# Performance work log

Hardware: AMD Instinct MI355X
Metric: run time of the kernel (lower is better)

The kernel has to match this reference:

```python
import jax, jax.numpy as jnp
import numpy as np
from jax import lax

N = 14
K = 512
NUM_CLASSES = 10
TAO = 0.5 / (N * N)
BETA = 2.0


def make_t_p(n=N, tao=TAO, beta=BETA):
    # t_p[i, j, a, b] = tao * max(1 - beta * (|a-i| + |b-j|) / n, -1)
    idx = jnp.arange(n, dtype=jnp.float32)
    d = (jnp.abs(idx[:, None, None, None] - idx[None, None, :, None])
         + jnp.abs(idx[None, :, None, None] - idx[None, None, None, :]))
    return (tao * jnp.maximum(1.0 - beta * d / n, -1.0)).astype(jnp.float32)


def masked_output(x, t_p):
    # Vectorized equivalent of computeMaskedOutput: global spatial argmax per
    # (batch, channel) selects a template, then masked = relu(x * template).
    B, H, W, C = x.shape
    flat_idx = jnp.argmax(x.reshape(B, H * W, C), axis=1)      # [B, C]
    pi, pj = flat_idx // W, flat_idx % W
    tpl = t_p[pi, pj]                                          # [B, C, H, W]
    tpl = jnp.transpose(tpl, (0, 2, 3, 1))                     # [B, H, W, C]
    masked = jax.nn.relu(x * tpl)
    return masked, x, tpl


def compute_loss(x, pos_templates, act_sums, cls_sums, gt):
    # Fused segment-sum form of the original nested python loops.
    classes = jnp.zeros(NUM_CLASSES, x.dtype).at[gt].add(1.0)  # bincount
    cls_new = cls_sums + classes
    means = jnp.mean(x, axis=(1, 2))                           # [B, C]
    onehot = jax.nn.one_hot(gt, NUM_CLASSES, dtype=x.dtype)    # [B, 10]
    act_new = act_sums + means.T @ onehot                      # [C, 10]
    # divide_no_nan
    fm = jnp.where(cls_new[None, :] == 0, 0.0,
                   act_new / jnp.where(cls_new[None, :] == 0, 1.0, cls_new[None, :]))
    fclass = jnp.argmax(fm, axis=1)                            # [C]
    match = fclass[None, :] == gt[:, None]                     # [B, C]
    pt = jax.nn.relu(pos_templates)
    # relu(t_n) == 0 since t_n is strictly negative
    loss = jnp.where(match[:, None, None, :], pt, 0.0)
    return loss, act_new, cls_new


def forward(inputs, gt, conv_w, conv_b, dense_w, dense_b,
            activation_sums_1, activation_sums_2, class_sums_1, class_sums_2):
    t_p = make_t_p()
    raw_map = inputs  # base_model treated as identity on its feature map
    x1, X1_relu, pos_t1 = masked_output(raw_map, t_p)
    x3 = jax.nn.relu(lax.conv_general_dilated(
        x1, conv_w, window_strides=(1, 1), padding='SAME',
        dimension_numbers=('NHWC', 'HWIO', 'NHWC')) + conv_b)
    x2, X2_relu, pos_t2 = masked_output(x3, t_p)
    pooled = lax.reduce_window(x2, -jnp.inf, lax.max,
                               (1, 2, 2, 1), (1, 2, 2, 1), 'VALID')
    flat = pooled.reshape(pooled.shape[0], -1)
    probs = jax.nn.softmax(flat @ dense_w + dense_b, axis=-1)
    loss1, as1, cs1 = compute_loss(x1, pos_t1, activation_sums_1, class_sums_1, gt)
    loss2, as2, cs2 = compute_loss(x2, pos_t2, activation_sums_2, class_sums_2, gt)
    return probs, x1, x2, loss1, loss2, raw_map, pos_t1


def setup_inputs() -> dict:
    key = jax.random.key(0)
    ks = jax.random.split(key, 4)
    B = 128
    inputs = jax.random.uniform(ks[0], (B, N, N, K), dtype=jnp.float32)
    gt = jax.random.randint(ks[1], (B,), 0, NUM_CLASSES)
    conv_w = jax.random.normal(ks[2], (3, 3, K, K), dtype=jnp.float32) * 0.02
    conv_b = jnp.zeros((K,), jnp.float32)
    D = (N // 2) * (N // 2) * K  # 25088
    dense_w = jax.random.normal(ks[3], (D, NUM_CLASSES), dtype=jnp.float32) * 0.02
    dense_b = jnp.zeros((NUM_CLASSES,), jnp.float32)
    return {
        'inputs': inputs, 'gt': gt,
        'conv_w': conv_w, 'conv_b': conv_b,
        'dense_w': dense_w, 'dense_b': dense_b,
        'activation_sums_1': jnp.zeros((K, NUM_CLASSES), jnp.float32),
        'activation_sums_2': jnp.zeros((K, NUM_CLASSES), jnp.float32),
        'class_sums_1': jnp.zeros((NUM_CLASSES,), jnp.float32),
        'class_sums_2': jnp.zeros((NUM_CLASSES,), jnp.float32),
    }


def reference(inputs, gt, conv_w, conv_b, dense_w, dense_b,
              activation_sums_1, activation_sums_2, class_sums_1, class_sums_2):
    return forward(inputs, gt, conv_w, conv_b, dense_w, dense_b,
                   activation_sums_1, activation_sums_2,
                   class_sums_1, class_sums_2)
```

## Files before the change

kernel.cpp:

```cpp
#include <hip/hip_runtime.h>
#include <hip/hip_bf16.h>
#include <stdint.h>

#define TAO_F (0.5f/196.0f)

typedef short s16x8 __attribute__((ext_vector_type(8)));
typedef float f32x4 __attribute__((ext_vector_type(4)));
typedef __attribute__((address_space(1))) const unsigned int u32_g;
typedef __attribute__((address_space(3))) unsigned int u32_l;

__device__ __forceinline__ void async_ld16(const void* g, void* l) {
  __builtin_amdgcn_global_load_lds((u32_g*)g, (u32_l*)l, 16, 0, 0);
}

__global__ void k_prep_w(const float* __restrict__ w, __hip_bfloat16* __restrict__ wT) {
  __shared__ float tile[64][65];
  int bid = blockIdx.x;
  int r = bid / 64; int rem = bid - r * 64;
  int cib = (rem >> 3) * 64, cob = (rem & 7) * 64;
  int tid = threadIdx.x;
  int col = tid & 63, rw = tid >> 6;
#pragma unroll
  for (int p = 0; p < 16; ++p) {
    int row = p * 4 + rw;
    tile[row][col] = w[(size_t)(r * 512 + cib + row) * 512 + cob + col];
  }
  __syncthreads();
#pragma unroll
  for (int p = 0; p < 16; ++p) {
    int row = p * 4 + rw;
    wT[(size_t)(r * 512 + cob + row) * 512 + cib + col] = __float2bfloat16(tile[col][row]);
  }
}

__global__ void k_argmax(const float* __restrict__ src, int* __restrict__ idx,
                         float* __restrict__ rawcopy) {
  int t = blockIdx.x * 256 + threadIdx.x;
  const float* p = src + (size_t)(t >> 9) * 196 * 512 + (t & 511);
  float best = -1e30f; int bi = 0;
  if (rawcopy) {
    float* rp = rawcopy + (size_t)(t >> 9) * 196 * 512 + (t & 511);
    for (int s = 0; s < 196; ++s) {
      float v = p[(size_t)s * 512];
      rp[(size_t)s * 512] = v;
      if (v > best) { best = v; bi = s; }
    }
  } else {
    for (int s = 0; s < 196; ++s) {
      float v = p[(size_t)s * 512];
      if (v > best) { best = v; bi = s; }
    }
  }
  idx[t] = bi;
}

__global__ void k_mask1(const float* __restrict__ in, const int* __restrict__ idx1,
                        const int* __restrict__ gt, float* __restrict__ out_x1,
                        float* __restrict__ out_t1, __hip_bfloat16* __restrict__ x1p,
                        float* __restrict__ act1) {
  int t = blockIdx.x * 256 + threadIdx.x;
  int b = t >> 9, c = t & 511;
  int id = idx1[t];
  int pi = id / 14, pj = id - pi * 14;
  const float* ip = in + (size_t)b * 196 * 512 + c;
  float* ox = out_x1 + (size_t)b * 196 * 512 + c;
  float* ot = out_t1 + (size_t)b * 196 * 512 + c;
  __hip_bfloat16* xp = x1p + ((size_t)(b * 16 + 1) * 16 + 1) * 512 + c;
  float sum = 0.f;
  for (int i = 0; i < 14; ++i) {
    int di = (i > pi) ? (i - pi) : (pi - i);
    for (int j = 0; j < 14; ++j) {
      int d = di + ((j > pj) ? (j - pj) : (pj - j));
      float tpl = TAO_F * fmaxf(1.0f - (float)d / 7.0f, -1.0f);
      float x = ip[(size_t)(i * 14 + j) * 512];
      float m = fmaxf(x * tpl, 0.0f);
      ox[(size_t)(i * 14 + j) * 512] = m;
      ot[(size_t)(i * 14 + j) * 512] = tpl;
      xp[(size_t)(i * 16 + j) * 512] = __float2bfloat16(m);
      sum += m;
    }
  }
  atomicAdd(&act1[c * 10 + gt[b]], sum * (1.0f / 196.0f));
}

__global__ void k_mask2(const float* __restrict__ x3, const int* __restrict__ idx2,
                        const int* __restrict__ gt, float* __restrict__ out_x2,
                        float* __restrict__ act2) {
  int t = blockIdx.x * 256 + threadIdx.x;
  int b = t >> 9, c = t & 511;
  int id = idx2[t];
  int pi = id / 14, pj = id - pi * 14;
  const float* ip = x3 + (size_t)b * 196 * 512 + c;
  float* ox = out_x2 + (size_t)b * 196 * 512 + c;
  float sum = 0.f;
  for (int i = 0; i < 14; ++i) {
    int di = (i > pi) ? (i - pi) : (pi - i);
    for (int j = 0; j < 14; ++j) {
      int d = di + ((j > pj) ? (j - pj) : (pj - j));
      float tpl = TAO_F * fmaxf(1.0f - (float)d / 7.0f, -1.0f);
      float x = ip[(size_t)(i * 14 + j) * 512];
      float m = fmaxf(x * tpl, 0.0f);
      ox[(size_t)(i * 14 + j) * 512] = m;
      sum += m;
    }
  }
  atomicAdd(&act2[c * 10 + gt[b]], sum * (1.0f / 196.0f));
}

__global__ __launch_bounds__(256, 2) void k_gemm(const __hip_bfloat16* __restrict__ x1p,
                                                 const __hip_bfloat16* __restrict__ wT,
                                                 const float* __restrict__ conv_b,
                                                 float* __restrict__ x3) {
  int bid = blockIdx.x;
  int nt4 = bid & 3; int mt196 = bid >> 2;
  int m0 = mt196 * 128, co0 = nt4 * 128;
  int tid = threadIdx.x;
  int lane = tid & 63;

  __shared__ short As[128 * 64];
  __shared__ short Bs[128 * 64];

  int srow = tid >> 3;
  int sslot = tid & 7;
  int sx = ((sslot ^ (srow & 7)) * 8);

  int baseA[4];
#pragma unroll
  for (int p = 0; p < 4; ++p) {
    int m = m0 + p * 32 + srow;
    int b = m / 196; int s = m - b * 196; int i = s / 14; int j = s - i * 14;
    baseA[p] = ((b * 16 + i + 1) * 16 + (j + 1)) * 512;
  }
  int baseB[4];
#pragma unroll
  for (int p = 0; p < 4; ++p) baseB[p] = (co0 + p * 32 + srow) * 512;

  f32x4 acc[4][4] = {};

  int m_off = (tid >> 7) * 64;
  int n_off = ((tid >> 6) & 1) * 64;
  int q = lane >> 4;
  int l16 = lane & 15;

  for (int r = 0; r < 9; ++r) {
    int offr = ((r / 3) * 16 + (r % 3) - 17) * 512;
    int wbase = r * 512 * 512;
    for (int cb = 0; cb < 8; ++cb) {
      int ko = cb * 64;
      __syncthreads();
#pragma unroll
      for (int p = 0; p < 4; ++p) {
        async_ld16(x1p + (baseA[p] + offr + ko + sx),
                   &As[(p * 32 + srow) * 64 + sslot * 8]);
        async_ld16(wT + (wbase + baseB[p] + ko + sx),
                   &Bs[(p * 32 + srow) * 64 + sslot * 8]);
      }
      __syncthreads();
#pragma unroll
      for (int kk = 0; kk < 2; ++kk) {
        s16x8 af[4], bf[4];
#pragma unroll
        for (int tt = 0; tt < 4; ++tt) {
          int rowa = m_off + tt * 16 + l16;
          int sa = (kk * 4 + q) ^ (rowa & 7);
          af[tt] = *(const s16x8*)&As[rowa * 64 + sa * 8];
          int rowb = n_off + tt * 16 + l16;
          int sb = (kk * 4 + q) ^ (rowb & 7);
          bf[tt] = *(const s16x8*)&Bs[rowb * 64 + sb * 8];
        }
#pragma unroll
        for (int mt = 0; mt < 4; ++mt)
#pragma unroll
          for (int nt = 0; nt < 4; ++nt)
            acc[mt][nt] = __builtin_amdgcn_mfma_f32_16x16x32_bf16(af[mt], bf[nt], acc[mt][nt], 0, 0, 0);
      }
    }
  }
#pragma unroll
  for (int nt = 0; nt < 4; ++nt) {
    int col = co0 + n_off + nt * 16 + l16;
    float bias = conv_b[col];
#pragma unroll
    for (int mt = 0; mt < 4; ++mt) {
      int mrow = m0 + m_off + mt * 16 + q * 4;
#pragma unroll
      for (int rg = 0; rg < 4; ++rg) {
        float v = acc[mt][nt][rg] + bias;
        x3[(size_t)(mrow + rg) * 512 + col] = fmaxf(v, 0.0f);
      }
    }
  }
}

__global__ void k_dense(const float* __restrict__ x2, const float* __restrict__ dw,
                        const float* __restrict__ db, float* __restrict__ probs) {
  int b = blockIdx.x, tid = threadIdx.x;
  float a[10] = {0.f,0.f,0.f,0.f,0.f,0.f,0.f,0.f,0.f,0.f};
  for (int d = tid; d < 25088; d += 256) {
    int c = d & 511;
    int sj = d >> 9;
    int ii = sj / 7, jj = sj - ii * 7;
    const float* xb = x2 + ((size_t)(b * 14 + 2 * ii) * 14 + 2 * jj) * 512 + c;
    float p0 = xb[0], p1 = xb[512], p2 = xb[14 * 512], p3 = xb[14 * 512 + 512];
    float pm = fmaxf(fmaxf(p0, p1), fmaxf(p2, p3));
    const float* wr = dw + (size_t)d * 10;
#pragma unroll
    for (int t2 = 0; t2 < 10; ++t2) a[t2] += pm * wr[t2];
  }
  __shared__ float red[10];
  if (tid < 10) red[tid] = 0.f;
  __syncthreads();
  int lane = tid & 63;
#pragma unroll
  for (int t2 = 0; t2 < 10; ++t2) {
    float v = a[t2];
    for (int off = 32; off > 0; off >>= 1) v += __shfl_down(v, off);
    if (lane == 0) atomicAdd(&red[t2], v);
  }
  __syncthreads();
  if (tid == 0) {
    float l[10]; float m = -1e30f;
#pragma unroll
    for (int t2 = 0; t2 < 10; ++t2) { l[t2] = red[t2] + db[t2]; m = fmaxf(m, l[t2]); }
    float s = 0.f;
#pragma unroll
    for (int t2 = 0; t2 < 10; ++t2) { l[t2] = expf(l[t2] - m); s += l[t2]; }
    float inv = 1.0f / s;
#pragma unroll
    for (int t2 = 0; t2 < 10; ++t2) probs[b * 10 + t2] = l[t2] * inv;
  }
}

__global__ void k_stats(const float* __restrict__ act1, const float* __restrict__ act2,
                        const float* __restrict__ as1, const float* __restrict__ as2,
                        const float* __restrict__ cs1, const float* __restrict__ cs2,
                        const int* __restrict__ gt, int* __restrict__ fc1, int* __restrict__ fc2) {
  __shared__ int scnt[10];
  int tid = threadIdx.x;
  if (tid < 10) scnt[tid] = 0;
  __syncthreads();
  if (tid < 128) atomicAdd(&scnt[gt[tid]], 1);
  __syncthreads();
  int c = tid;
  float best1 = -1e30f, best2 = -1e30f; int b1 = 0, b2 = 0;
#pragma unroll
  for (int g = 0; g < 10; ++g) {
    float cnt = (float)scnt[g];
    float cn1 = cs1[g] + cnt;
    float cn2 = cs2[g] + cnt;
    float a1 = act1[c * 10 + g] + as1[c * 10 + g];
    float a2 = act2[c * 10 + g] + as2[c * 10 + g];
    float f1 = (cn1 == 0.f) ? 0.f : a1 / cn1;
    float f2 = (cn2 == 0.f) ? 0.f : a2 / cn2;
    if (f1 > best1) { best1 = f1; b1 = g; }
    if (f2 > best2) { best2 = f2; b2 = g; }
  }
  fc1[c] = b1; fc2[c] = b2;
}

__global__ void k_loss(const int* __restrict__ idx1, const int* __restrict__ idx2,
                       const int* __restrict__ fc1, const int* __restrict__ fc2,
                       const int* __restrict__ gt, float* __restrict__ o1, float* __restrict__ o2) {
  int t = blockIdx.x * 256 + threadIdx.x;
  int b = t >> 9, c = t & 511;
  int g = gt[b];
  bool m1 = (fc1[c] == g), m2 = (fc2[c] == g);
  int i1 = idx1[t], i2 = idx2[t];
  int p1i = i1 / 14, p1j = i1 - p1i * 14;
  int p2i = i2 / 14, p2j = i2 - p2i * 14;
  float* w1 = o1 + (size_t)b * 196 * 512 + c;
  float* w2 = o2 + (size_t)b * 196 * 512 + c;
  for (int i = 0; i < 14; ++i) {
    int d1i = (i > p1i) ? (i - p1i) : (p1i - i);
    int d2i = (i > p2i) ? (i - p2i) : (p2i - i);
    for (int j = 0; j < 14; ++j) {
      int d1 = d1i + ((j > p1j) ? (j - p1j) : (p1j - j));
      int d2 = d2i + ((j > p2j) ? (j - p2j) : (p2j - j));
      float r1 = TAO_F * fmaxf(1.0f - (float)d1 / 7.0f, 0.0f);
      float r2 = TAO_F * fmaxf(1.0f - (float)d2 / 7.0f, 0.0f);
      w1[(size_t)(i * 14 + j) * 512] = m1 ? r1 : 0.0f;
      w2[(size_t)(i * 14 + j) * 512] = m2 ? r2 : 0.0f;
    }
  }
}

extern "C" void kernel_launch(void* const* d_in, const int* in_sizes, int n_in,
                              void* d_out, int out_size, void* d_ws, size_t ws_size,
                              hipStream_t stream) {
  const float* inputs  = (const float*)d_in[0];
  const int*   gt      = (const int*)d_in[1];
  const float* conv_w  = (const float*)d_in[2];
  const float* conv_b  = (const float*)d_in[3];
  const float* dense_w = (const float*)d_in[4];
  const float* dense_b = (const float*)d_in[5];
  const float* as1     = (const float*)d_in[6];
  const float* as2     = (const float*)d_in[7];
  const float* cs1     = (const float*)d_in[8];
  const float* cs2     = (const float*)d_in[9];

  float* out = (float*)d_out;
  const size_t S = 12845056;
  float* o_probs = out;
  float* o_x1  = out + 1280;
  float* o_x2  = o_x1 + S;
  float* o_l1  = o_x2 + S;
  float* o_l2  = o_l1 + S;
  float* o_raw = o_l2 + S;
  float* o_t1  = o_raw + S;

  uint8_t* w8 = (uint8_t*)d_ws;
  __hip_bfloat16* x1p = (__hip_bfloat16*)w8;
  float* x3  = (float*)(w8 + 33554432);
  __hip_bfloat16* wT = (__hip_bfloat16*)(w8 + 84934656);
  int*   idx1 = (int*)(w8 + 89653248);
  int*   idx2 = (int*)(w8 + 89915392);
  float* act1 = (float*)(w8 + 90177536);
  float* act2 = (float*)(w8 + 90198016);
  int*   fc1  = (int*)(w8 + 90218496);
  int*   fc2  = (int*)(w8 + 90220544);

  hipMemsetAsync(x1p, 0, 33554432, stream);
  hipMemsetAsync(act1, 0, 40960, stream);

  k_prep_w<<<576, 256, 0, stream>>>(conv_w, wT);
  k_argmax<<<256, 256, 0, stream>>>(inputs, idx1, o_raw);
  k_mask1 <<<256, 256, 0, stream>>>(inputs, idx1, gt, o_x1, o_t1, x1p, act1);
  k_gemm  <<<784, 256, 0, stream>>>(x1p, wT, conv_b, x3);
  k_argmax<<<256, 256, 0, stream>>>(x3, idx2, nullptr);
  k_mask2 <<<256, 256, 0, stream>>>(x3, idx2, gt, o_x2, act2);
  k_dense <<<128, 256, 0, stream>>>(o_x2, dense_w, dense_b, o_probs);
  k_stats <<<1, 512, 0, stream>>>(act1, act2, as1, as2, cs1, cs2, gt, fc1, fc2);
  k_loss  <<<256, 256, 0, stream>>>(idx1, idx2, fc1, fc2, gt, o_l1, o_l2);
}
```

Measured before the change: 671.3 us.

## Fuse argmax with masking and fold dense layer into second mask pass

Merges the argmax and masking kernels for both stages so each thread scans its channel column once for the argmax and then re-reads it for the mask, avoiding a separate launch and idx round-trip. The second fused kernel also does the 2x2 maxpool and dense matvec in registers, accumulating logits atomically so o_x2 is never re-read. Softmax moves into k_stats, and the GEMM launch bound is raised to 3 blocks per SM, which may force register spills. Dense weights are now read per channel-thread with stride-10 access, and float atomics on logits make the summation order nondeterministic.

After: 623.9 us. -7.1%, faster.

```diff
diff --git a/kernel.cpp b/kernel.cpp
--- a/kernel.cpp
+++ b/kernel.cpp
@@ -33,38 +33,24 @@
   }
 }
 
-__global__ void k_argmax(const float* __restrict__ src, int* __restrict__ idx,
-                         float* __restrict__ rawcopy) {
-  int t = blockIdx.x * 256 + threadIdx.x;
-  const float* p = src + (size_t)(t >> 9) * 196 * 512 + (t & 511);
-  float best = -1e30f; int bi = 0;
-  if (rawcopy) {
-    float* rp = rawcopy + (size_t)(t >> 9) * 196 * 512 + (t & 511);
-    for (int s = 0; s < 196; ++s) {
-      float v = p[(size_t)s * 512];
-      rp[(size_t)s * 512] = v;
-      if (v > best) { best = v; bi = s; }
-    }
-  } else {
-    for (int s = 0; s < 196; ++s) {
-      float v = p[(size_t)s * 512];
-      if (v > best) { best = v; bi = s; }
-    }
-  }
-  idx[t] = bi;
-}
-
-__global__ void k_mask1(const float* __restrict__ in, const int* __restrict__ idx1,
-                        const int* __restrict__ gt, float* __restrict__ out_x1,
-                        float* __restrict__ out_t1, __hip_bfloat16* __restrict__ x1p,
-                        float* __restrict__ act1) {
+__global__ void k_fuse1(const float* __restrict__ in, const int* __restrict__ gt,
+                        float* __restrict__ o_raw, float* __restrict__ o_x1,
+                        float* __restrict__ o_t1, __hip_bfloat16* __restrict__ x1p,
+                        float* __restrict__ act1, int* __restrict__ idx1) {
   int t = blockIdx.x * 256 + threadIdx.x;
   int b = t >> 9, c = t & 511;
-  int id = idx1[t];
-  int pi = id / 14, pj = id - pi * 14;
   const float* ip = in + (size_t)b * 196 * 512 + c;
-  float* ox = out_x1 + (size_t)b * 196 * 512 + c;
-  float* ot = out_t1 + (size_t)b * 196 * 512 + c;
+  float* rp = o_raw + (size_t)b * 196 * 512 + c;
+  float best = -1e30f; int bi = 0;
+  for (int s = 0; s < 196; ++s) {
+    float v = ip[(size_t)s * 512];
+    rp[(size_t)s * 512] = v;
+    if (v > best) { best = v; bi = s; }
+  }
+  idx1[t] = bi;
+  int pi = bi / 14, pj = bi - pi * 14;
+  float* ox = o_x1 + (size_t)b * 196 * 512 + c;
+  float* ot = o_t1 + (size_t)b * 196 * 512 + c;
   __hip_bfloat16* xp = x1p + ((size_t)(b * 16 + 1) * 16 + 1) * 512 + c;
   float sum = 0.f;
   for (int i = 0; i < 14; ++i) {
@@ -83,31 +69,7 @@
   atomicAdd(&act1[c * 10 + gt[b]], sum * (1.0f / 196.0f));
 }
 
-__global__ void k_mask2(const float* __restrict__ x3, const int* __restrict__ idx2,
-                        const int* __restrict__ gt, float* __restrict__ out_x2,
-                        float* __restrict__ act2) {
-  int t = blockIdx.x * 256 + threadIdx.x;
-  int b = t >> 9, c = t & 511;
-  int id = idx2[t];
-  int pi = id / 14, pj = id - pi * 14;
-  const float* ip = x3 + (size_t)b * 196 * 512 + c;
-  float* ox = out_x2 + (size_t)b * 196 * 512 + c;
-  float sum = 0.f;
-  for (int i = 0; i < 14; ++i) {
-    int di = (i > pi) ? (i - pi) : (pi - i);
-    for (int j = 0; j < 14; ++j) {
-      int d = di + ((j > pj) ? (j - pj) : (pj - j));
-      float tpl = TAO_F * fmaxf(1.0f - (float)d / 7.0f, -1.0f);
-      float x = ip[(size_t)(i * 14 + j) * 512];
-      float m = fmaxf(x * tpl, 0.0f);
-      ox[(size_t)(i * 14 + j) * 512] = m;
-      sum += m;
-    }
-  }
-  atomicAdd(&act2[c * 10 + gt[b]], sum * (1.0f / 196.0f));
-}
-
-__global__ __launch_bounds__(256, 2) void k_gemm(const __hip_bfloat16* __restrict__ x1p,
+__global__ __launch_bounds__(256, 3) void k_gemm(const __hip_bfloat16* __restrict__ x1p,
                                                  const __hip_bfloat16* __restrict__ wT,
                                                  const float* __restrict__ conv_b,
                                                  float* __restrict__ x3) {
@@ -192,25 +154,54 @@
   }
 }
 
-__global__ void k_dense(const float* __restrict__ x2, const float* __restrict__ dw,
-                        const float* __restrict__ db, float* __restrict__ probs) {
-  int b = blockIdx.x, tid = threadIdx.x;
+__global__ void k_fuse2(const float* __restrict__ x3, const int* __restrict__ gt,
+                        const float* __restrict__ dw, float* __restrict__ o_x2,
+                        float* __restrict__ act2, float* __restrict__ logits,
+                        int* __restrict__ idx2) {
+  int t = blockIdx.x * 256 + threadIdx.x;
+  int b = t >> 9, c = t & 511;
+  const float* ip = x3 + (size_t)b * 196 * 512 + c;
+  float best = -1e30f; int bi = 0;
+  for (int s = 0; s < 196; ++s) {
+    float v = ip[(size_t)s * 512];
+    if (v > best) { best = v; bi = s; }
+  }
+  idx2[t] = bi;
+  int pi = bi / 14, pj = bi - pi * 14;
+  float* ox = o_x2 + (size_t)b * 196 * 512 + c;
+  float sum = 0.f;
   float a[10] = {0.f,0.f,0.f,0.f,0.f,0.f,0.f,0.f,0.f,0.f};
-  for (int d = tid; d < 25088; d += 256) {
-    int c = d & 511;
-    int sj = d >> 9;
-    int ii = sj / 7, jj = sj - ii * 7;
-    const float* xb = x2 + ((size_t)(b * 14 + 2 * ii) * 14 + 2 * jj) * 512 + c;
-    float p0 = xb[0], p1 = xb[512], p2 = xb[14 * 512], p3 = xb[14 * 512 + 512];
-    float pm = fmaxf(fmaxf(p0, p1), fmaxf(p2, p3));
-    const float* wr = dw + (size_t)d * 10;
-#pragma unroll
-    for (int t2 = 0; t2 < 10; ++t2) a[t2] += pm * wr[t2];
-  }
+  for (int ii = 0; ii < 7; ++ii) {
+    float rv[2][14];
+#pragma unroll
+    for (int r2 = 0; r2 < 2; ++r2) {
+      int i = 2 * ii + r2;
+      int di = (i > pi) ? (i - pi) : (pi - i);
+#pragma unroll
+      for (int j = 0; j < 14; ++j) {
+        int d = di + ((j > pj) ? (j - pj) : (pj - j));
+        float tpl = TAO_F * fmaxf(1.0f - (float)d / 7.0f, -1.0f);
+        float x = ip[(size_t)(i * 14 + j) * 512];
+        float m = fmaxf(x * tpl, 0.0f);
+        ox[(size_t)(i * 14 + j) * 512] = m;
+        sum += m;
+        rv[r2][j] = m;
+      }
+    }
+#pragma unroll
+    for (int jj = 0; jj < 7; ++jj) {
+      float pm = fmaxf(fmaxf(rv[0][2 * jj], rv[0][2 * jj + 1]),
+                       fmaxf(rv[1][2 * jj], rv[1][2 * jj + 1]));
+      const float* wr = dw + ((size_t)((ii * 7 + jj) * 512 + c)) * 10;
+#pragma unroll
+      for (int t2 = 0; t2 < 10; ++t2) a[t2] += pm * wr[t2];
+    }
+  }
+  atomicAdd(&act2[c * 10 + gt[b]], sum * (1.0f / 196.0f));
   __shared__ float red[10];
-  if (tid < 10) red[tid] = 0.f;
-  __syncthreads();
-  int lane = tid & 63;
+  if (threadIdx.x < 10) red[threadIdx.x] = 0.f;
+  __syncthreads();
+  int lane = threadIdx.x & 63;
 #pragma unroll
   for (int t2 = 0; t2 < 10; ++t2) {
     float v = a[t2];
@@ -218,23 +209,15 @@
     if (lane == 0) atomicAdd(&red[t2], v);
   }
   __syncthreads();
-  if (tid == 0) {
-    float l[10]; float m = -1e30f;
-#pragma unroll
-    for (int t2 = 0; t2 < 10; ++t2) { l[t2] = red[t2] + db[t2]; m = fmaxf(m, l[t2]); }
-    float s = 0.f;
-#pragma unroll
-    for (int t2 = 0; t2 < 10; ++t2) { l[t2] = expf(l[t2] - m); s += l[t2]; }
-    float inv = 1.0f / s;
-#pragma unroll
-    for (int t2 = 0; t2 < 10; ++t2) probs[b * 10 + t2] = l[t2] * inv;
-  }
+  if (threadIdx.x < 10) atomicAdd(&logits[b * 10 + threadIdx.x], red[threadIdx.x]);
 }
 
 __global__ void k_stats(const float* __restrict__ act1, const float* __restrict__ act2,
                         const float* __restrict__ as1, const float* __restrict__ as2,
                         const float* __restrict__ cs1, const float* __restrict__ cs2,
-                        const int* __restrict__ gt, int* __restrict__ fc1, int* __restrict__ fc2) {
+                        const int* __restrict__ gt, const float* __restrict__ logits,
+                        const float* __restrict__ db, int* __restrict__ fc1,
+                        int* __restrict__ fc2, float* __restrict__ o_probs) {
   __shared__ int scnt[10];
   int tid = threadIdx.x;
   if (tid < 10) scnt[tid] = 0;
@@ -256,6 +239,17 @@
     if (f2 > best2) { best2 = f2; b2 = g; }
   }
   fc1[c] = b1; fc2[c] = b2;
+  if (tid < 128) {
+    float l[10]; float m = -1e30f;
+#pragma unroll
+    for (int t2 = 0; t2 < 10; ++t2) { l[t2] = logits[tid * 10 + t2] + db[t2]; m = fmaxf(m, l[t2]); }
+    float s = 0.f;
+#pragma unroll
+    for (int t2 = 0; t2 < 10; ++t2) { l[t2] = expf(l[t2] - m); s += l[t2]; }
+    float inv = 1.0f / s;
+#pragma unroll
+    for (int t2 = 0; t2 < 10; ++t2) o_probs[tid * 10 + t2] = l[t2] * inv;
+  }
 }
 
 __global__ void k_loss(const int* __restrict__ idx1, const int* __restrict__ idx2,
@@ -316,19 +310,18 @@
   int*   idx2 = (int*)(w8 + 89915392);
   float* act1 = (float*)(w8 + 90177536);
   float* act2 = (float*)(w8 + 90198016);
-  int*   fc1  = (int*)(w8 + 90218496);
-  int*   fc2  = (int*)(w8 + 90220544);
+  float* logits = (float*)(w8 + 90218496);
+  int*   fc1  = (int*)(w8 + 90223616);
+  int*   fc2  = (int*)(w8 + 90225664);
 
   hipMemsetAsync(x1p, 0, 33554432, stream);
-  hipMemsetAsync(act1, 0, 40960, stream);
+  hipMemsetAsync(act1, 0, 46080, stream);
 
   k_prep_w<<<576, 256, 0, stream>>>(conv_w, wT);
-  k_argmax<<<256, 256, 0, stream>>>(inputs, idx1, o_raw);
-  k_mask1 <<<256, 256, 0, stream>>>(inputs, idx1, gt, o_x1, o_t1, x1p, act1);
+  k_fuse1 <<<256, 256, 0, stream>>>(inputs, gt, o_raw, o_x1, o_t1, x1p, act1, idx1);
   k_gemm  <<<784, 256, 0, stream>>>(x1p, wT, conv_b, x3);
-  k_argmax<<<256, 256, 0, stream>>>(x3, idx2, nullptr);
-  k_mask2 <<<256, 256, 0, stream>>>(x3, idx2, gt, o_x2, act2);
-  k_dense <<<128, 256, 0, stream>>>(o_x2, dense_w, dense_b, o_probs);
-  k_stats <<<1, 512, 0, stream>>>(act1, act2, as1, as2, cs1, cs2, gt, fc1, fc2);
+  k_fuse2 <<<256, 256, 0, stream>>>(x3, gt, dense_w, o_x2, act2, logits, idx2);
+  k_stats <<<1, 512, 0, stream>>>(act1, act2, as1, as2, cs1, cs2, gt, logits, dense_b,
+                                  fc1, fc2, o_probs);
   k_loss  <<<256, 256, 0, stream>>>(idx1, idx2, fc1, fc2, gt, o_l1, o_l2);
 }
```
